# Optimization experiments

Measured on AMD Instinct MI355X. Metric: run time of the kernel, lower is better.

Reference implementation:

```python
import jax, jax.numpy as jnp
import numpy as np

VQ_NUM = 3
EMB_NUM = 1024
COMMITMENT_WEIGHT = 1.0
# cumprod of [1, emb_num, emb_num] -> per-stage index bases
CUMPROD = [1, EMB_NUM, EMB_NUM * EMB_NUM]


def setup_inputs() -> dict:
    key = jax.random.key(0)
    k0, k1, k2, k3 = jax.random.split(key, 4)
    z = jax.random.normal(k0, (8, 4096, 512), dtype=jnp.float32)
    # linear_in: nn.Linear(in_ch=512, emb_ch=256, bias=False) -> weight [emb_ch, in_ch]
    W_in = jax.random.normal(k1, (VQ_NUM, 256, 512), dtype=jnp.float32) * 0.02
    # linear_out: nn.Linear(emb_ch=256, in_ch=512, bias=False) -> weight [in_ch, emb_ch]
    W_out = jax.random.normal(k2, (VQ_NUM, 512, 256), dtype=jnp.float32) * 0.02
    # one codebook per stage (share_residual_codebooks=False)
    codebooks = jax.random.normal(k3, (VQ_NUM, EMB_NUM, 256), dtype=jnp.float32) * 0.02
    return {"z": z, "W_in": W_in, "W_out": W_out, "codebooks": codebooks}


def reference(z, W_in, W_out, codebooks):
    sg = jax.lax.stop_gradient
    z_q = jnp.zeros_like(z)
    r = z
    loss = jnp.float32(0.0)
    index_sum = jnp.zeros(z.shape[:2], dtype=jnp.int64 if jax.config.jax_enable_x64 else jnp.int32)
    for i in range(VQ_NUM):
        # linear_in
        zi = jnp.einsum('bnc,ec->bne', r, W_in[i])  # [B,N,emb_ch]
        v = codebooks[i]  # [S, emb_ch]
        # squared L2 distance: ||z||^2 + ||v||^2 - 2 z.v
        dist = (jnp.sum(zi * zi, axis=-1, keepdims=True)
                + jnp.sum(v * v, axis=-1)
                - 2.0 * jnp.einsum('bne,se->bns', zi, v))  # [B,N,S]
        idx = jnp.argmin(dist, axis=-1)  # [B,N] int
        zq = v[idx]  # codebook lookup, [B,N,emb_ch]
        loss = loss + (COMMITMENT_WEIGHT * jnp.mean((sg(zq) - zi) ** 2)
                       + jnp.mean((zq - sg(zi)) ** 2))
        # straight-through estimator
        zq_ste = zi + sg(zq - zi)
        # linear_out
        r_q = jnp.einsum('bne,ce->bnc', zq_ste, W_out[i])  # [B,N,in_ch]
        index_sum = index_sum + idx.astype(index_sum.dtype) * CUMPROD[i]
        z_q = z_q + r_q
        r = z - sg(z_q)
    loss = loss / VQ_NUM + jnp.mean((z_q - z) ** 2)
    return z_q, index_sum, loss
```

## Files before the change

### kernel.cpp

```cpp
#include <hip/hip_runtime.h>

#define MTOK 32768
#define CIN  512
#define EMB  256
#define NCODE 1024
#define VQ   3
#define DELTA 2e-3f

typedef short s16x8 __attribute__((ext_vector_type(8)));
typedef float f32x4 __attribute__((ext_vector_type(4)));
typedef unsigned short u16;

static __device__ __forceinline__ u16 f2bf(float x) {
    unsigned int u = __float_as_uint(x);
    u += 0x7FFF + ((u >> 16) & 1);
    return (u16)(u >> 16);
}
static __device__ __forceinline__ float bf2f(u16 h) {
    return __uint_as_float(((unsigned int)h) << 16);
}

__global__ void init_k(double* loss_acc, int* cnt) {
    loss_acc[0] = 0.0;
    loss_acc[1] = 0.0;
    cnt[0] = 0; cnt[1] = 0; cnt[2] = 0;
}

__global__ __launch_bounds__(64) void prep_cb_k(const float* __restrict__ cbs,
                                                double* __restrict__ vnorm64,
                                                float* __restrict__ vnorm32,
                                                u16* __restrict__ cbh,
                                                u16* __restrict__ cbl) {
    int s = blockIdx.x;
    const float* row = cbs + (size_t)s * EMB;
    double acc = 0.0;
    for (int k = threadIdx.x; k < EMB; k += 64) {
        float v = row[k];
        double vd = (double)v; acc += vd * vd;
        u16 h = f2bf(v);
        u16 l = f2bf(v - bf2f(h));
        cbh[(size_t)s * EMB + k] = h;
        cbl[(size_t)s * EMB + k] = l;
    }
    #pragma unroll
    for (int off = 32; off > 0; off >>= 1) acc += __shfl_down(acc, off, 64);
    if (threadIdx.x == 0) { vnorm64[s] = acc; vnorm32[s] = (float)acc; }
}

__global__ __launch_bounds__(256) void prep_w_k(const float* __restrict__ W_in,
                                                u16* __restrict__ wh,
                                                u16* __restrict__ wl) {
    int i = blockIdx.x * 256 + threadIdx.x;
    float v = W_in[i];
    u16 h = f2bf(v);
    wh[i] = h;
    wl[i] = f2bf(v - bf2f(h));
}

__global__ __launch_bounds__(256) void prep_T_k(const float* __restrict__ cbs,
                                                const float* __restrict__ Wout,
                                                float* __restrict__ T) {
    const int stage = blockIdx.z;
    const float* A = cbs  + (size_t)stage * NCODE * EMB;
    const float* B = Wout + (size_t)stage * CIN * EMB;
    float* C = T + (size_t)stage * NCODE * CIN;
    __shared__ float As[64][33];
    __shared__ float Bs[64][33];
    const int tid = threadIdx.x;
    const int ty = tid >> 4, tx = tid & 15;
    const int m0 = blockIdx.x * 64;
    const int n0 = blockIdx.y * 64;
    const int lrow = tid >> 5, lcol = tid & 31;
    double acc[4][4];
    #pragma unroll
    for (int i = 0; i < 4; ++i)
        #pragma unroll
        for (int j = 0; j < 4; ++j) acc[i][j] = 0.0;

    for (int k0 = 0; k0 < EMB; k0 += 32) {
        __syncthreads();
        #pragma unroll
        for (int t = 0; t < 8; ++t) {
            int r = lrow + 8 * t;
            As[r][lcol] = A[(size_t)(m0 + r) * EMB + k0 + lcol];
            Bs[r][lcol] = B[(size_t)(n0 + r) * EMB + k0 + lcol];
        }
        __syncthreads();
        #pragma unroll
        for (int k = 0; k < 32; ++k) {
            double a[4], b[4];
            #pragma unroll
            for (int i = 0; i < 4; ++i) a[i] = (double)As[ty * 4 + i][k];
            #pragma unroll
            for (int j = 0; j < 4; ++j) b[j] = (double)Bs[tx * 4 + j][k];
            #pragma unroll
            for (int i = 0; i < 4; ++i)
                #pragma unroll
                for (int j = 0; j < 4; ++j) acc[i][j] += a[i] * b[j];
        }
    }
    #pragma unroll
    for (int i = 0; i < 4; ++i) {
        float4 v = make_float4((float)acc[i][0], (float)acc[i][1],
                               (float)acc[i][2], (float)acc[i][3]);
        *reinterpret_cast<float4*>(&C[(size_t)(m0 + ty * 4 + i) * CIN + n0 + tx * 4]) = v;
    }
}

__global__ __launch_bounds__(256, 2) void zi_mfma_k(const float* __restrict__ z,
                                                    const float* __restrict__ zq,
                                                    const u16* __restrict__ wh,
                                                    const u16* __restrict__ wl,
                                                    float* __restrict__ zi,
                                                    double* __restrict__ loss_acc,
                                                    int stage0) {
    __shared__ __align__(16) u16 swh[16][520];
    __shared__ __align__(16) u16 swl[16][520];
    const int tid = threadIdx.x;
    const int w = tid >> 6;
    const int l = tid & 63;
    const int col = l & 15;
    const int g = l >> 4;
    const int mw = blockIdx.x * 64 + w * 16;
    const int sr = tid >> 4, sq = tid & 15;

    s16x8 ah[16], al[16];
    {
        const float* zr = z  + (size_t)(mw + col) * CIN + g * 8;
        const float* qr = zq + (size_t)(mw + col) * CIN + g * 8;
        #pragma unroll
        for (int kc = 0; kc < 16; ++kc) {
            float4 f0 = *reinterpret_cast<const float4*>(zr + kc * 32);
            float4 f1 = *reinterpret_cast<const float4*>(zr + kc * 32 + 4);
            float f[8] = {f0.x, f0.y, f0.z, f0.w, f1.x, f1.y, f1.z, f1.w};
            if (!stage0) {
                float4 q0 = *reinterpret_cast<const float4*>(qr + kc * 32);
                float4 q1 = *reinterpret_cast<const float4*>(qr + kc * 32 + 4);
                f[0] -= q0.x; f[1] -= q0.y; f[2] -= q0.z; f[3] -= q0.w;
                f[4] -= q1.x; f[5] -= q1.y; f[6] -= q1.z; f[7] -= q1.w;
            }
            #pragma unroll
            for (int j = 0; j < 8; ++j) {
                u16 h = f2bf(f[j]);
                u16 lo = f2bf(f[j] - bf2f(h));
                ah[kc][j] = (short)h; al[kc][j] = (short)lo;
            }
        }
    }

    const u16* gh = wh + (size_t)sr * CIN + sq * 8;
    const u16* gl = wl + (size_t)sr * CIN + sq * 8;
    uint4 h0, h1, h2, h3, l0, l1, l2, l3;
    h0 = *(const uint4*)(gh);        h1 = *(const uint4*)(gh + 128);
    h2 = *(const uint4*)(gh + 256);  h3 = *(const uint4*)(gh + 384);
    l0 = *(const uint4*)(gl);        l1 = *(const uint4*)(gl + 128);
    l2 = *(const uint4*)(gl + 256);  l3 = *(const uint4*)(gl + 384);
    *(uint4*)&swh[sr][sq * 8]       = h0;  *(uint4*)&swh[sr][sq * 8 + 128] = h1;
    *(uint4*)&swh[sr][sq * 8 + 256] = h2;  *(uint4*)&swh[sr][sq * 8 + 384] = h3;
    *(uint4*)&swl[sr][sq * 8]       = l0;  *(uint4*)&swl[sr][sq * 8 + 128] = l1;
    *(uint4*)&swl[sr][sq * 8 + 256] = l2;  *(uint4*)&swl[sr][sq * 8 + 384] = l3;

    double zn = 0.0;
    for (int nt = 0; nt < 16; ++nt) {
        __syncthreads();
        if (nt < 15) {
            const u16* th = gh + (size_t)(nt + 1) * (16 * CIN);
            const u16* tl = gl + (size_t)(nt + 1) * (16 * CIN);
            h0 = *(const uint4*)(th);        h1 = *(const uint4*)(th + 128);
            h2 = *(const uint4*)(th + 256);  h3 = *(const uint4*)(th + 384);
            l0 = *(const uint4*)(tl);        l1 = *(const uint4*)(tl + 128);
            l2 = *(const uint4*)(tl + 256);  l3 = *(const uint4*)(tl + 384);
        }
        f32x4 a0 = {0.f, 0.f, 0.f, 0.f};
        f32x4 a1 = {0.f, 0.f, 0.f, 0.f};
        f32x4 a2 = {0.f, 0.f, 0.f, 0.f};
        #pragma unroll
        for (int kc = 0; kc < 16; ++kc) {
            s16x8 Bh = *(const s16x8*)&swh[col][g * 8 + kc * 32];
            s16x8 Bl = *(const s16x8*)&swl[col][g * 8 + kc * 32];
            a0 = __builtin_amdgcn_mfma_f32_16x16x32_bf16(ah[kc], Bh, a0, 0, 0, 0);
            a1 = __builtin_amdgcn_mfma_f32_16x16x32_bf16(al[kc], Bh, a1, 0, 0, 0);
            a2 = __builtin_amdgcn_mfma_f32_16x16x32_bf16(ah[kc], Bl, a2, 0, 0, 0);
        }
        #pragma unroll
        for (int r = 0; r < 4; ++r) {
            float v = a0[r] + a1[r] + a2[r];
            zi[(size_t)(mw + g * 4 + r) * EMB + nt * 16 + col] = v;
            zn += (double)v * (double)v;
        }
        __syncthreads();
        if (nt < 15) {
            *(uint4*)&swh[sr][sq * 8]       = h0;  *(uint4*)&swh[sr][sq * 8 + 128] = h1;
            *(uint4*)&swh[sr][sq * 8 + 256] = h2;  *(uint4*)&swh[sr][sq * 8 + 384] = h3;
            *(uint4*)&swl[sr][sq * 8]       = l0;  *(uint4*)&swl[sr][sq * 8 + 128] = l1;
            *(uint4*)&swl[sr][sq * 8 + 256] = l2;  *(uint4*)&swl[sr][sq * 8 + 384] = l3;
        }
    }
    #pragma unroll
    for (int off = 32; off > 0; off >>= 1) zn += __shfl_down(zn, off, 64);
    if (l == 0) atomicAdd(loss_acc, zn);
}

__global__ __launch_bounds__(256, 2) void pref_k(const float* __restrict__ zi,
                                                 const u16* __restrict__ cbh,
                                                 const u16* __restrict__ cbl,
                                                 const float* __restrict__ vnorm32,
                                                 int* __restrict__ idx,
                                                 int* __restrict__ idx_sum,
                                                 float* __restrict__ mind,
                                                 int* __restrict__ flagged,
                                                 int* __restrict__ cnt,
                                                 double* __restrict__ loss_acc,
                                                 int stage0, int cumprod) {
    __shared__ __align__(16) u16 sbh[16][264];
    __shared__ __align__(16) u16 sbl[16][264];
    __shared__ double loss_s[16];
    const int tid = threadIdx.x;
    const int w = tid >> 6;
    const int l = tid & 63;
    const int col = l & 15;
    const int g = l >> 4;
    const int mw = blockIdx.x * 64 + w * 16;
    const int sr = tid >> 4, sq = tid & 15;

    s16x8 ah[8], al[8];
    {
        const float* zr = zi + (size_t)(mw + col) * EMB + g * 8;
        #pragma unroll
        for (int kc = 0; kc < 8; ++kc) {
            float4 f0 = *reinterpret_cast<const float4*>(zr + kc * 32);
            float4 f1 = *reinterpret_cast<const float4*>(zr + kc * 32 + 4);
            float f[8] = {f0.x, f0.y, f0.z, f0.w, f1.x, f1.y, f1.z, f1.w};
            #pragma unroll
            for (int j = 0; j < 8; ++j) {
                u16 h = f2bf(f[j]);
                u16 lo = f2bf(f[j] - bf2f(h));
                ah[kc][j] = (short)h;
                al[kc][j] = (short)lo;
            }
        }
    }

    float b1[4] = {1e30f, 1e30f, 1e30f, 1e30f};
    float b2[4] = {1e30f, 1e30f, 1e30f, 1e30f};
    int   i1[4] = {0, 0, 0, 0};

    const u16* gh = cbh + (size_t)sr * EMB + sq * 8;
    const u16* gl = cbl + (size_t)sr * EMB + sq * 8;
    uint4 h0, h1, l0, l1;
    h0 = *(const uint4*)(gh);  h1 = *(const uint4*)(gh + 128);
    l0 = *(const uint4*)(gl);  l1 = *(const uint4*)(gl + 128);
    *(uint4*)&sbh[sr][sq * 8]       = h0;  *(uint4*)&sbh[sr][sq * 8 + 128] = h1;
    *(uint4*)&sbl[sr][sq * 8]       = l0;  *(uint4*)&sbl[sr][sq * 8 + 128] = l1;

    for (int ct = 0; ct < 64; ++ct) {
        __syncthreads();
        if (ct < 63) {
            const u16* th = gh + (size_t)(ct + 1) * (16 * EMB);
            const u16* tl = gl + (size_t)(ct + 1) * (16 * EMB);
            h0 = *(const uint4*)(th);  h1 = *(const uint4*)(th + 128);
            l0 = *(const uint4*)(tl);  l1 = *(const uint4*)(tl + 128);
        }
        const float vn = vnorm32[ct * 16 + col];
        f32x4 a0 = {0.f, 0.f, 0.f, 0.f};
        f32x4 a1 = {0.f, 0.f, 0.f, 0.f};
        f32x4 a2 = {0.f, 0.f, 0.f, 0.f};
        #pragma unroll
        for (int kc = 0; kc < 8; ++kc) {
            s16x8 Bh = *(const s16x8*)&sbh[col][g * 8 + kc * 32];
            s16x8 Bl = *(const s16x8*)&sbl[col][g * 8 + kc * 32];
            a0 = __builtin_amdgcn_mfma_f32_16x16x32_bf16(ah[kc], Bh, a0, 0, 0, 0);
            a1 = __builtin_amdgcn_mfma_f32_16x16x32_bf16(al[kc], Bh, a1, 0, 0, 0);
            a2 = __builtin_amdgcn_mfma_f32_16x16x32_bf16(ah[kc], Bl, a2, 0, 0, 0);
        }
        #pragma unroll
        for (int r = 0; r < 4; ++r) {
            float sc = vn - 2.f * (a0[r] + a1[r] + a2[r]);
            if (sc < b1[r]) { b2[r] = b1[r]; b1[r] = sc; i1[r] = ct * 16 + col; }
            else b2[r] = fminf(b2[r], sc);
        }
        __syncthreads();
        if (ct < 63) {
            *(uint4*)&sbh[sr][sq * 8]       = h0;  *(uint4*)&sbh[sr][sq * 8 + 128] = h1;
            *(uint4*)&sbl[sr][sq * 8]       = l0;  *(uint4*)&sbl[sr][sq * 8 + 128] = l1;
        }
    }

    #pragma unroll
    for (int off = 1; off < 16; off <<= 1) {
        #pragma unroll
        for (int r = 0; r < 4; ++r) {
            float ob1 = __shfl_xor(b1[r], off, 64);
            int   oi1 = __shfl_xor(i1[r], off, 64);
            float ob2 = __shfl_xor(b2[r], off, 64);
            if (ob1 < b1[r] || (ob1 == b1[r] && oi1 < i1[r])) {
                b2[r] = fminf(b1[r], ob2); b1[r] = ob1; i1[r] = oi1;
            } else {
                b2[r] = fminf(b2[r], ob1);
            }
        }
    }
    if (col == 0) {
        double lsum = 0.0;
        #pragma unroll
        for (int r = 0; r < 4; ++r) {
            int m = mw + g * 4 + r;
            idx[m] = i1[r];
            if (stage0) idx_sum[m] = i1[r];
            else        idx_sum[m] += i1[r] * cumprod;
            mind[m] = b1[r];
            lsum += (double)b1[r];
            if (b2[r] - b1[r] < DELTA) {
                int slot = atomicAdd(cnt, 1);
                flagged[slot] = m;
            }
        }
        loss_s[w * 4 + g] = lsum;
    }
    __syncthreads();
    if (tid == 0) {
        double s = 0.0;
        #pragma unroll
        for (int q = 0; q < 16; ++q) s += loss_s[q];
        atomicAdd(loss_acc, s);
    }
}

__global__ __launch_bounds__(256) void rescan_k(const float* __restrict__ z,
                                                const float* __restrict__ zqv,
                                                const float* __restrict__ Win,
                                                const float* __restrict__ cb,
                                                const double* __restrict__ vnorm64,
                                                const int* __restrict__ flagged,
                                                const int* __restrict__ cnt,
                                                int* __restrict__ idx,
                                                int* __restrict__ idx_sum,
                                                float* __restrict__ mind,
                                                double* __restrict__ loss_acc,
                                                int cumprod, int stage0) {
    __shared__ double r64[CIN];
    __shared__ double zi64[EMB];
    __shared__ double sred[256];
    __shared__ int ired[256];
    int n = *cnt;
    for (int j = blockIdx.x; j < n; j += gridDim.x) {
        int m = flagged[j];
        __syncthreads();
        for (int k = threadIdx.x; k < CIN; k += 256) {
            float rv = z[(size_t)m * CIN + k];
            if (!stage0) rv -= zqv[(size_t)m * CIN + k];
            r64[k] = (double)rv;
        }
        __syncthreads();
        {
            const float* wr = Win + (size_t)threadIdx.x * CIN;
            double s = 0.0;
            for (int k = 0; k < CIN; ++k) s += r64[k] * (double)wr[k];
            zi64[threadIdx.x] = s;
        }
        __syncthreads();
        double best = 1e300; int bi = 0;
        for (int jj = 0; jj < 4; ++jj) {
            int c = threadIdx.x * 4 + jj;
            const float* row = cb + (size_t)c * EMB;
            double d = 0.0;
            for (int k = 0; k < EMB; ++k) d += zi64[k] * (double)row[k];
            double sc = vnorm64[c] - 2.0 * d;
            if (sc < best) { best = sc; bi = c; }
        }
        sred[threadIdx.x] = best; ired[threadIdx.x] = bi;
        __syncthreads();
        for (int off = 128; off > 0; off >>= 1) {
            if (threadIdx.x < off) {
                double ob = sred[threadIdx.x + off]; int oi = ired[threadIdx.x + off];
                if (ob < sred[threadIdx.x] ||
                    (ob == sred[threadIdx.x] && oi < ired[threadIdx.x])) {
                    sred[threadIdx.x] = ob; ired[threadIdx.x] = oi;
                }
            }
            __syncthreads();
        }
        if (threadIdx.x == 0) {
            int newI = ired[0], oldI = idx[m];
            if (newI != oldI) { idx[m] = newI; idx_sum[m] += (newI - oldI) * cumprod; }
            atomicAdd(loss_acc, sred[0] - (double)mind[m]);
            mind[m] = (float)sred[0];
        }
        __syncthreads();
    }
}

__global__ __launch_bounds__(256) void gather_k(const float* __restrict__ T,
                                                const int* __restrict__ idx,
                                                const float* __restrict__ z,
                                                float* __restrict__ zq,
                                                int stage0, int last,
                                                double* __restrict__ loss_acc) {
    __shared__ double red[256];
    int m = blockIdx.x * 16 + (threadIdx.x >> 4);
    int q = threadIdx.x & 15;
    const float* src = T + (size_t)idx[m] * CIN;
    float* dst = zq + (size_t)m * CIN;
    double s = 0.0;
    #pragma unroll
    for (int it = 0; it < 8; ++it) {
        int off = it * 64 + q * 4;
        float4 t = *reinterpret_cast<const float4*>(src + off);
        if (!stage0) {
            float4 o = *reinterpret_cast<const float4*>(dst + off);
            t.x += o.x; t.y += o.y; t.z += o.z; t.w += o.w;
        }
        *reinterpret_cast<float4*>(dst + off) = t;
        if (last) {
            float4 zv = *reinterpret_cast<const float4*>(z + (size_t)m * CIN + off);
            double d0 = (double)zv.x - (double)t.x;
            double d1 = (double)zv.y - (double)t.y;
            double d2 = (double)zv.z - (double)t.z;
            double d3 = (double)zv.w - (double)t.w;
            s += d0 * d0 + d1 * d1 + d2 * d2 + d3 * d3;
        }
    }
    if (last) {
        red[threadIdx.x] = s;
        __syncthreads();
        for (int off = 128; off > 0; off >>= 1) {
            if (threadIdx.x < off) red[threadIdx.x] += red[threadIdx.x + off];
            __syncthreads();
        }
        if (threadIdx.x == 0) atomicAdd(loss_acc + 1, red[0]);
    }
}

__global__ void final_k(const int* __restrict__ idx_sum,
                        const double* __restrict__ loss_acc,
                        float* __restrict__ out) {
    int i = blockIdx.x * blockDim.x + threadIdx.x;
    if (i < MTOK) out[MTOK * CIN + i] = (float)idx_sum[i];
    if (i == 0) {
        double loss = 2.0 * loss_acc[0] / (3.0 * (double)MTOK * (double)EMB)
                    + loss_acc[1] / ((double)MTOK * (double)CIN);
        out[MTOK * CIN + MTOK] = (float)loss;
    }
}

extern "C" void kernel_launch(void* const* d_in, const int* in_sizes, int n_in,
                              void* d_out, int out_size, void* d_ws, size_t ws_size,
                              hipStream_t stream) {
    const float* z     = (const float*)d_in[0];
    const float* W_in  = (const float*)d_in[1];
    const float* W_out = (const float*)d_in[2];
    const float* cbs   = (const float*)d_in[3];
    float* out = (float*)d_out;
    char* ws = (char*)d_ws;

    double* vnorm64  = (double*)ws;
    double* loss_acc = (double*)(ws + 24576);
    float*  vnorm32  = (float*)(ws + 24592);
    int*    cnt      = (int*)(ws + 36880);
    u16*    cbh      = (u16*)(ws + 36896);
    u16*    cbl      = (u16*)(ws + 1609760);
    u16*    wh       = (u16*)(ws + 3182624);
    u16*    wl       = (u16*)(ws + 3969056);
    float*  T        = (float*)(ws + 4755488);
    float*  zi       = (float*)(ws + 11046944);
    char*   p        = ws + 11046944 + (size_t)MTOK * EMB * 4;
    int*    idx      = (int*)p;
    int*    idx_sum  = (int*)(p + 131072);
    int*    flagged  = (int*)(p + 262144);
    float*  mind     = (float*)(p + 393216);

    float* zq = out;

    init_k<<<dim3(1), dim3(1), 0, stream>>>(loss_acc, cnt);
    prep_cb_k<<<dim3(VQ * NCODE), dim3(64), 0, stream>>>(cbs, vnorm64, vnorm32, cbh, cbl);
    prep_w_k<<<dim3(VQ * EMB * CIN / 256), dim3(256), 0, stream>>>(W_in, wh, wl);
    prep_T_k<<<dim3(NCODE / 64, CIN / 64, VQ), dim3(256), 0, stream>>>(cbs, W_out, T);

    const int cumprod[VQ] = {1, 1024, 1024 * 1024};
    for (int i = 0; i < VQ; ++i) {
        const float* cb = cbs + (size_t)i * NCODE * EMB;
        zi_mfma_k<<<dim3(MTOK / 64), dim3(256), 0, stream>>>(
            z, zq, wh + (size_t)i * EMB * CIN, wl + (size_t)i * EMB * CIN,
            zi, loss_acc, i == 0 ? 1 : 0);
        pref_k<<<dim3(MTOK / 64), dim3(256), 0, stream>>>(
            zi, cbh + (size_t)i * NCODE * EMB, cbl + (size_t)i * NCODE * EMB,
            vnorm32 + i * NCODE, idx, idx_sum, mind, flagged, cnt + i, loss_acc,
            i == 0 ? 1 : 0, cumprod[i]);
        rescan_k<<<dim3(512), dim3(256), 0, stream>>>(
            z, zq, W_in + (size_t)i * EMB * CIN, cb, vnorm64 + i * NCODE,
            flagged, cnt + i, idx, idx_sum, mind, loss_acc, cumprod[i],
            i == 0 ? 1 : 0);
        gather_k<<<dim3(MTOK / 16), dim3(256), 0, stream>>>(
            T + (size_t)i * NCODE * CIN, idx, z, zq, i == 0 ? 1 : 0,
            i == VQ - 1 ? 1 : 0, loss_acc);
    }
    final_k<<<dim3(MTOK / 256), dim3(256), 0, stream>>>(idx_sum, loss_acc, out);
}
```

Measured before the change: 951.1 us.

## Double-buffer LDS tiles and narrow rescan to top-two candidates when gap allows

Both MFMA kernels now use double-buffered shared tiles, so each iteration needs one barrier instead of two. The prefilter tracks the top three scores and the second-best index, and flags rows as needing a full rescan only when the third-best is also within the margin. Otherwise the rescan compares just the two candidates in double precision. The rescan kernel is also restructured into wave-level dot products with shuffle reductions instead of thread-per-output loops with shared-memory reductions. This adds register pressure in the prefilter and an extra cand2 buffer.

```diff
diff --git a/kernel.cpp b/kernel.cpp
--- a/kernel.cpp
+++ b/kernel.cpp
@@ -114,8 +114,8 @@
                                                     float* __restrict__ zi,
                                                     double* __restrict__ loss_acc,
                                                     int stage0) {
-    __shared__ __align__(16) u16 swh[16][520];
-    __shared__ __align__(16) u16 swl[16][520];
+    __shared__ __align__(16) u16 swh[2][16][520];
+    __shared__ __align__(16) u16 swl[2][16][520];
     const int tid = threadIdx.x;
     const int w = tid >> 6;
     const int l = tid & 63;
@@ -151,33 +151,33 @@
     const u16* gh = wh + (size_t)sr * CIN + sq * 8;
     const u16* gl = wl + (size_t)sr * CIN + sq * 8;
     uint4 h0, h1, h2, h3, l0, l1, l2, l3;
-    h0 = *(const uint4*)(gh);        h1 = *(const uint4*)(gh + 128);
-    h2 = *(const uint4*)(gh + 256);  h3 = *(const uint4*)(gh + 384);
-    l0 = *(const uint4*)(gl);        l1 = *(const uint4*)(gl + 128);
-    l2 = *(const uint4*)(gl + 256);  l3 = *(const uint4*)(gl + 384);
-    *(uint4*)&swh[sr][sq * 8]       = h0;  *(uint4*)&swh[sr][sq * 8 + 128] = h1;
-    *(uint4*)&swh[sr][sq * 8 + 256] = h2;  *(uint4*)&swh[sr][sq * 8 + 384] = h3;
-    *(uint4*)&swl[sr][sq * 8]       = l0;  *(uint4*)&swl[sr][sq * 8 + 128] = l1;
-    *(uint4*)&swl[sr][sq * 8 + 256] = l2;  *(uint4*)&swl[sr][sq * 8 + 384] = l3;
+#define ZLOAD(NT) do { const u16* th = gh + (size_t)(NT) * (16 * CIN);                \
+    const u16* tl = gl + (size_t)(NT) * (16 * CIN);                                   \
+    h0 = *(const uint4*)(th);        h1 = *(const uint4*)(th + 128);                  \
+    h2 = *(const uint4*)(th + 256);  h3 = *(const uint4*)(th + 384);                  \
+    l0 = *(const uint4*)(tl);        l1 = *(const uint4*)(tl + 128);                  \
+    l2 = *(const uint4*)(tl + 256);  l3 = *(const uint4*)(tl + 384); } while (0)
+#define ZWRITE(P) do {                                                                \
+    *(uint4*)&swh[P][sr][sq * 8]       = h0;  *(uint4*)&swh[P][sr][sq * 8 + 128] = h1;\
+    *(uint4*)&swh[P][sr][sq * 8 + 256] = h2;  *(uint4*)&swh[P][sr][sq * 8 + 384] = h3;\
+    *(uint4*)&swl[P][sr][sq * 8]       = l0;  *(uint4*)&swl[P][sr][sq * 8 + 128] = l1;\
+    *(uint4*)&swl[P][sr][sq * 8 + 256] = l2;  *(uint4*)&swl[P][sr][sq * 8 + 384] = l3;\
+    } while (0)
+    ZLOAD(0); ZWRITE(0); ZLOAD(1);
 
     double zn = 0.0;
     for (int nt = 0; nt < 16; ++nt) {
         __syncthreads();
-        if (nt < 15) {
-            const u16* th = gh + (size_t)(nt + 1) * (16 * CIN);
-            const u16* tl = gl + (size_t)(nt + 1) * (16 * CIN);
-            h0 = *(const uint4*)(th);        h1 = *(const uint4*)(th + 128);
-            h2 = *(const uint4*)(th + 256);  h3 = *(const uint4*)(th + 384);
-            l0 = *(const uint4*)(tl);        l1 = *(const uint4*)(tl + 128);
-            l2 = *(const uint4*)(tl + 256);  l3 = *(const uint4*)(tl + 384);
-        }
+        const int p = nt & 1;
+        if (nt + 1 < 16) ZWRITE((nt + 1) & 1);
+        if (nt + 2 < 16) ZLOAD(nt + 2);
         f32x4 a0 = {0.f, 0.f, 0.f, 0.f};
         f32x4 a1 = {0.f, 0.f, 0.f, 0.f};
         f32x4 a2 = {0.f, 0.f, 0.f, 0.f};
         #pragma unroll
         for (int kc = 0; kc < 16; ++kc) {
-            s16x8 Bh = *(const s16x8*)&swh[col][g * 8 + kc * 32];
-            s16x8 Bl = *(const s16x8*)&swl[col][g * 8 + kc * 32];
+            s16x8 Bh = *(const s16x8*)&swh[p][col][g * 8 + kc * 32];
+            s16x8 Bl = *(const s16x8*)&swl[p][col][g * 8 + kc * 32];
             a0 = __builtin_amdgcn_mfma_f32_16x16x32_bf16(ah[kc], Bh, a0, 0, 0, 0);
             a1 = __builtin_amdgcn_mfma_f32_16x16x32_bf16(al[kc], Bh, a1, 0, 0, 0);
             a2 = __builtin_amdgcn_mfma_f32_16x16x32_bf16(ah[kc], Bl, a2, 0, 0, 0);
@@ -188,14 +188,9 @@
             zi[(size_t)(mw + g * 4 + r) * EMB + nt * 16 + col] = v;
             zn += (double)v * (double)v;
         }
-        __syncthreads();
-        if (nt < 15) {
-            *(uint4*)&swh[sr][sq * 8]       = h0;  *(uint4*)&swh[sr][sq * 8 + 128] = h1;
-            *(uint4*)&swh[sr][sq * 8 + 256] = h2;  *(uint4*)&swh[sr][sq * 8 + 384] = h3;
-            *(uint4*)&swl[sr][sq * 8]       = l0;  *(uint4*)&swl[sr][sq * 8 + 128] = l1;
-            *(uint4*)&swl[sr][sq * 8 + 256] = l2;  *(uint4*)&swl[sr][sq * 8 + 384] = l3;
-        }
-    }
+    }
+#undef ZLOAD
+#undef ZWRITE
     #pragma unroll
     for (int off = 32; off > 0; off >>= 1) zn += __shfl_down(zn, off, 64);
     if (l == 0) atomicAdd(loss_acc, zn);
@@ -210,10 +205,11 @@
                                                  float* __restrict__ mind,
                                                  int* __restrict__ flagged,
                                                  int* __restrict__ cnt,
+                                                 int* __restrict__ cand2,
                                                  double* __restrict__ loss_acc,
                                                  int stage0, int cumprod) {
-    __shared__ __align__(16) u16 sbh[16][264];
-    __shared__ __align__(16) u16 sbl[16][264];
+    __shared__ __align__(16) u16 sbh[2][16][264];
+    __shared__ __align__(16) u16 sbl[2][16][264];
     __shared__ double loss_s[16];
     const int tid = threadIdx.x;
     const int w = tid >> 6;
@@ -243,32 +239,36 @@
 
     float b1[4] = {1e30f, 1e30f, 1e30f, 1e30f};
     float b2[4] = {1e30f, 1e30f, 1e30f, 1e30f};
+    float b3[4] = {1e30f, 1e30f, 1e30f, 1e30f};
     int   i1[4] = {0, 0, 0, 0};
+    int   i2[4] = {0, 0, 0, 0};
 
     const u16* gh = cbh + (size_t)sr * EMB + sq * 8;
     const u16* gl = cbl + (size_t)sr * EMB + sq * 8;
     uint4 h0, h1, l0, l1;
-    h0 = *(const uint4*)(gh);  h1 = *(const uint4*)(gh + 128);
-    l0 = *(const uint4*)(gl);  l1 = *(const uint4*)(gl + 128);
-    *(uint4*)&sbh[sr][sq * 8]       = h0;  *(uint4*)&sbh[sr][sq * 8 + 128] = h1;
-    *(uint4*)&sbl[sr][sq * 8]       = l0;  *(uint4*)&sbl[sr][sq * 8 + 128] = l1;
+#define PLOAD(CT) do { const u16* th = gh + (size_t)(CT) * (16 * EMB);                \
+    const u16* tl = gl + (size_t)(CT) * (16 * EMB);                                   \
+    h0 = *(const uint4*)(th);  h1 = *(const uint4*)(th + 128);                        \
+    l0 = *(const uint4*)(tl);  l1 = *(const uint4*)(tl + 128); } while (0)
+#define PWRITE(P) do {                                                                \
+    *(uint4*)&sbh[P][sr][sq * 8] = h0;  *(uint4*)&sbh[P][sr][sq * 8 + 128] = h1;      \
+    *(uint4*)&sbl[P][sr][sq * 8] = l0;  *(uint4*)&sbl[P][sr][sq * 8 + 128] = l1;      \
+    } while (0)
+    PLOAD(0); PWRITE(0); PLOAD(1);
 
     for (int ct = 0; ct < 64; ++ct) {
         __syncthreads();
-        if (ct < 63) {
-            const u16* th = gh + (size_t)(ct + 1) * (16 * EMB);
-            const u16* tl = gl + (size_t)(ct + 1) * (16 * EMB);
-            h0 = *(const uint4*)(th);  h1 = *(const uint4*)(th + 128);
-            l0 = *(const uint4*)(tl);  l1 = *(const uint4*)(tl + 128);
-        }
+        const int p = ct & 1;
+        if (ct + 1 < 64) PWRITE((ct + 1) & 1);
+        if (ct + 2 < 64) PLOAD(ct + 2);
         const float vn = vnorm32[ct * 16 + col];
         f32x4 a0 = {0.f, 0.f, 0.f, 0.f};
         f32x4 a1 = {0.f, 0.f, 0.f, 0.f};
         f32x4 a2 = {0.f, 0.f, 0.f, 0.f};
         #pragma unroll
         for (int kc = 0; kc < 8; ++kc) {
-            s16x8 Bh = *(const s16x8*)&sbh[col][g * 8 + kc * 32];
-            s16x8 Bl = *(const s16x8*)&sbl[col][g * 8 + kc * 32];
+            s16x8 Bh = *(const s16x8*)&sbh[p][col][g * 8 + kc * 32];
+            s16x8 Bl = *(const s16x8*)&sbl[p][col][g * 8 + kc * 32];
             a0 = __builtin_amdgcn_mfma_f32_16x16x32_bf16(ah[kc], Bh, a0, 0, 0, 0);
             a1 = __builtin_amdgcn_mfma_f32_16x16x32_bf16(al[kc], Bh, a1, 0, 0, 0);
             a2 = __builtin_amdgcn_mfma_f32_16x16x32_bf16(ah[kc], Bl, a2, 0, 0, 0);
@@ -276,28 +276,41 @@
         #pragma unroll
         for (int r = 0; r < 4; ++r) {
             float sc = vn - 2.f * (a0[r] + a1[r] + a2[r]);
-            if (sc < b1[r]) { b2[r] = b1[r]; b1[r] = sc; i1[r] = ct * 16 + col; }
-            else b2[r] = fminf(b2[r], sc);
-        }
-        __syncthreads();
-        if (ct < 63) {
-            *(uint4*)&sbh[sr][sq * 8]       = h0;  *(uint4*)&sbh[sr][sq * 8 + 128] = h1;
-            *(uint4*)&sbl[sr][sq * 8]       = l0;  *(uint4*)&sbl[sr][sq * 8 + 128] = l1;
-        }
-    }
+            int c = ct * 16 + col;
+            if (sc < b1[r]) { b3[r] = b2[r]; b2[r] = b1[r]; i2[r] = i1[r]; b1[r] = sc; i1[r] = c; }
+            else if (sc < b2[r]) { b3[r] = b2[r]; b2[r] = sc; i2[r] = c; }
+            else b3[r] = fminf(b3[r], sc);
+        }
+    }
+#undef PLOAD
+#undef PWRITE
 
     #pragma unroll
     for (int off = 1; off < 16; off <<= 1) {
         #pragma unroll
         for (int r = 0; r < 4; ++r) {
-            float ob1 = __shfl_xor(b1[r], off, 64);
-            int   oi1 = __shfl_xor(i1[r], off, 64);
-            float ob2 = __shfl_xor(b2[r], off, 64);
-            if (ob1 < b1[r] || (ob1 == b1[r] && oi1 < i1[r])) {
-                b2[r] = fminf(b1[r], ob2); b1[r] = ob1; i1[r] = oi1;
+            float c1 = __shfl_xor(b1[r], off, 64);
+            int   j1 = __shfl_xor(i1[r], off, 64);
+            float c2 = __shfl_xor(b2[r], off, 64);
+            int   j2 = __shfl_xor(i2[r], off, 64);
+            float c3 = __shfl_xor(b3[r], off, 64);
+            float nb1, nb2, nb3; int ni1, ni2;
+            if (c1 < b1[r] || (c1 == b1[r] && j1 < i1[r])) {
+                nb1 = c1; ni1 = j1;
+                if (b1[r] < c2 || (b1[r] == c2 && i1[r] < j2)) {
+                    nb2 = b1[r]; ni2 = i1[r]; nb3 = fminf(b2[r], c2);
+                } else {
+                    nb2 = c2; ni2 = j2; nb3 = fminf(b1[r], c3);
+                }
             } else {
-                b2[r] = fminf(b2[r], ob1);
-            }
+                nb1 = b1[r]; ni1 = i1[r];
+                if (c1 < b2[r] || (c1 == b2[r] && j1 < i2[r])) {
+                    nb2 = c1; ni2 = j1; nb3 = fminf(b2[r], c2);
+                } else {
+                    nb2 = b2[r]; ni2 = i2[r]; nb3 = fminf(c1, b3[r]);
+                }
+            }
+            b1[r] = nb1; b2[r] = nb2; b3[r] = nb3; i1[r] = ni1; i2[r] = ni2;
         }
     }
     if (col == 0) {
@@ -312,7 +325,9 @@
             lsum += (double)b1[r];
             if (b2[r] - b1[r] < DELTA) {
                 int slot = atomicAdd(cnt, 1);
-                flagged[slot] = m;
+                int full = (b3[r] - b1[r] < DELTA) ? 1 : 0;
+                flagged[slot] = (m << 1) | full;
+                cand2[m] = i2[r];
             }
         }
         loss_s[w * 4 + g] = lsum;
@@ -333,60 +348,97 @@
                                                 const double* __restrict__ vnorm64,
                                                 const int* __restrict__ flagged,
                                                 const int* __restrict__ cnt,
+                                                const int* __restrict__ cand2,
                                                 int* __restrict__ idx,
                                                 int* __restrict__ idx_sum,
                                                 float* __restrict__ mind,
                                                 double* __restrict__ loss_acc,
                                                 int cumprod, int stage0) {
-    __shared__ double r64[CIN];
     __shared__ double zi64[EMB];
-    __shared__ double sred[256];
-    __shared__ int ired[256];
+    __shared__ double sred[4];
+    __shared__ int ired[4];
+    const int tid = threadIdx.x;
+    const int w = tid >> 6, l = tid & 63;
     int n = *cnt;
     for (int j = blockIdx.x; j < n; j += gridDim.x) {
-        int m = flagged[j];
-        __syncthreads();
-        for (int k = threadIdx.x; k < CIN; k += 256) {
-            float rv = z[(size_t)m * CIN + k];
-            if (!stage0) rv -= zqv[(size_t)m * CIN + k];
-            r64[k] = (double)rv;
-        }
-        __syncthreads();
+        int fm = flagged[j];
+        int m = fm >> 1;
+        int full = fm & 1;
+        __syncthreads();
+        double rr[8];
         {
-            const float* wr = Win + (size_t)threadIdx.x * CIN;
+            const float* zr = z   + (size_t)m * CIN + l;
+            const float* qr = zqv + (size_t)m * CIN + l;
+            #pragma unroll
+            for (int jj = 0; jj < 8; ++jj) {
+                float rv = zr[64 * jj];
+                if (!stage0) rv -= qr[64 * jj];
+                rr[jj] = (double)rv;
+            }
+        }
+        for (int eo = 0; eo < 64; ++eo) {
+            int e = (w << 6) + eo;
+            const float* wr = Win + (size_t)e * CIN + l;
             double s = 0.0;
-            for (int k = 0; k < CIN; ++k) s += r64[k] * (double)wr[k];
-            zi64[threadIdx.x] = s;
-        }
-        __syncthreads();
-        double best = 1e300; int bi = 0;
-        for (int jj = 0; jj < 4; ++jj) {
-            int c = threadIdx.x * 4 + jj;
-            const float* row = cb + (size_t)c * EMB;
-            double d = 0.0;
-            for (int k = 0; k < EMB; ++k) d += zi64[k] * (double)row[k];
-            double sc = vnorm64[c] - 2.0 * d;
-            if (sc < best) { best = sc; bi = c; }
-        }
-        sred[threadIdx.x] = best; ired[threadIdx.x] = bi;
-        __syncthreads();
-        for (int off = 128; off > 0; off >>= 1) {
-            if (threadIdx.x < off) {
-                double ob = sred[threadIdx.x + off]; int oi = ired[threadIdx.x + off];
-                if (ob < sred[threadIdx.x] ||
-                    (ob == sred[threadIdx.x] && oi < ired[threadIdx.x])) {
-                    sred[threadIdx.x] = ob; ired[threadIdx.x] = oi;
-                }
-            }
+            #pragma unroll
+            for (int jj = 0; jj < 8; ++jj) s += rr[jj] * (double)wr[64 * jj];
+            #pragma unroll
+            for (int off = 1; off < 64; off <<= 1) s += __shfl_xor(s, off, 64);
+            if (l == 0) zi64[e] = s;
+        }
+        __syncthreads();
+        double z0 = zi64[4 * l], z1 = zi64[4 * l + 1];
+        double z2 = zi64[4 * l + 2], z3 = zi64[4 * l + 3];
+        if (full) {
+            double best = 1e300; int bi = 0;
+            for (int c = w; c < NCODE; c += 4) {
+                float4 v = *(const float4*)(cb + (size_t)c * EMB + 4 * l);
+                double s = z0 * (double)v.x + z1 * (double)v.y
+                         + z2 * (double)v.z + z3 * (double)v.w;
+                #pragma unroll
+                for (int off = 1; off < 64; off <<= 1) s += __shfl_xor(s, off, 64);
+                double sc = vnorm64[c] - 2.0 * s;
+                if (sc < best) { best = sc; bi = c; }
+            }
+            if (l == 0) { sred[w] = best; ired[w] = bi; }
             __syncthreads();
-        }
-        if (threadIdx.x == 0) {
-            int newI = ired[0], oldI = idx[m];
-            if (newI != oldI) { idx[m] = newI; idx_sum[m] += (newI - oldI) * cumprod; }
-            atomicAdd(loss_acc, sred[0] - (double)mind[m]);
-            mind[m] = (float)sred[0];
-        }
-        __syncthreads();
+            if (tid == 0) {
+                best = sred[0]; bi = ired[0];
+                for (int q = 1; q < 4; ++q)
+                    if (sred[q] < best || (sred[q] == best && ired[q] < bi)) {
+                        best = sred[q]; bi = ired[q];
+                    }
+                int oldI = idx[m];
+                if (bi != oldI) { idx[m] = bi; idx_sum[m] += (bi - oldI) * cumprod; }
+                atomicAdd(loss_acc, best - (double)mind[m]);
+                mind[m] = (float)best;
+            }
+        } else {
+            int cA = idx[m];
+            int cB = cand2[m];
+            float4 vA = *(const float4*)(cb + (size_t)cA * EMB + 4 * l);
+            float4 vB = *(const float4*)(cb + (size_t)cB * EMB + 4 * l);
+            double sA = z0 * (double)vA.x + z1 * (double)vA.y
+                      + z2 * (double)vA.z + z3 * (double)vA.w;
+            double sB = z0 * (double)vB.x + z1 * (double)vB.y
+                      + z2 * (double)vB.z + z3 * (double)vB.w;
+            #pragma unroll
+            for (int off = 1; off < 64; off <<= 1) {
+                sA += __shfl_xor(sA, off, 64);
+                sB += __shfl_xor(sB, off, 64);
+            }
+            if (tid == 0) {
+                double dA = vnorm64[cA] - 2.0 * sA;
+                double dB = vnorm64[cB] - 2.0 * sB;
+                int bi; double best;
+                if (dB < dA || (dB == dA && cB < cA)) { bi = cB; best = dB; }
+                else                                   { bi = cA; best = dA; }
+                int oldI = idx[m];
+                if (bi != oldI) { idx[m] = bi; idx_sum[m] += (bi - oldI) * cumprod; }
+                atomicAdd(loss_acc, best - (double)mind[m]);
+                mind[m] = (float)best;
+            }
+        }
     }
 }
 
@@ -468,6 +520,7 @@
     int*    idx_sum  = (int*)(p + 131072);
     int*    flagged  = (int*)(p + 262144);
     float*  mind     = (float*)(p + 393216);
+    int*    cand2    = (int*)(p + 524288);
 
     float* zq = out;
 
@@ -484,11 +537,11 @@
             zi, loss_acc, i == 0 ? 1 : 0);
         pref_k<<<dim3(MTOK / 64), dim3(256), 0, stream>>>(
             zi, cbh + (size_t)i * NCODE * EMB, cbl + (size_t)i * NCODE * EMB,
-            vnorm32 + i * NCODE, idx, idx_sum, mind, flagged, cnt + i, loss_acc,
-            i == 0 ? 1 : 0, cumprod[i]);
+            vnorm32 + i * NCODE, idx, idx_sum, mind, flagged, cnt + i, cand2,
+            loss_acc, i == 0 ? 1 : 0, cumprod[i]);
         rescan_k<<<dim3(512), dim3(256), 0, stream>>>(
             z, zq, W_in + (size_t)i * EMB * CIN, cb, vnorm64 + i * NCODE,
-            flagged, cnt + i, idx, idx_sum, mind, loss_acc, cumprod[i],
+            flagged, cnt + i, cand2, idx, idx_sum, mind, loss_acc, cumprod[i],
             i == 0 ? 1 : 0);
         gather_k<<<dim3(MTOK / 16), dim3(256), 0, stream>>>(
             T + (size_t)i * NCODE * CIN, idx, z, zq, i == 0 ? 1 : 0,
```

Result: slower. 1.177 ms (+23.7%).
